# Kernel optimization log

Measured on AMD Instinct MI355X. Metric: run time of the kernel, lower is better.

## Reference

```python
import jax, jax.numpy as jnp
import numpy as np

N_HEAD = 16
D_HEAD = 64
D_MODEL = 1024
QLEN = 1024
BSZ = 4
RLEN = 1024
CONV = 7
SCALE = 1.0 / D_HEAD ** 0.5
NEG = -1e30
EPS = 1e-5


def setup_inputs() -> dict:
    key = jax.random.key(0)
    ks = jax.random.split(key, 14)
    s = 0.02
    inp = {
        "w": jax.random.normal(ks[0], (QLEN, BSZ, D_MODEL), jnp.float32),
        "r": jax.random.normal(ks[1], (RLEN, D_MODEL), jnp.float32),
        "r_w_bias": jax.random.normal(ks[2], (N_HEAD, D_HEAD), jnp.float32) * s,
        "r_r_bias": jax.random.normal(ks[3], (N_HEAD, D_HEAD), jnp.float32) * s,
        "W_qkv": jax.random.normal(ks[4], (3 * N_HEAD * D_HEAD, D_MODEL), jnp.float32) * s,
        "W_r": jax.random.normal(ks[5], (N_HEAD * D_HEAD, D_MODEL), jnp.float32) * s,
        "W_o": jax.random.normal(ks[6], (D_MODEL, N_HEAD * D_HEAD), jnp.float32) * s,
        "conv_wq": jax.random.normal(ks[7], (D_HEAD, D_HEAD, CONV), jnp.float32) * s,
        "conv_bq": jax.random.normal(ks[8], (D_HEAD,), jnp.float32) * s,
        "conv_wk": jax.random.normal(ks[9], (D_HEAD, D_HEAD, CONV), jnp.float32) * s,
        "conv_bk": jax.random.normal(ks[10], (D_HEAD,), jnp.float32) * s,
        "conv_wv": jax.random.normal(ks[11], (D_HEAD, D_HEAD, CONV), jnp.float32) * s,
        "conv_bv": jax.random.normal(ks[12], (D_HEAD,), jnp.float32) * s,
        "ln_gamma": jnp.ones((D_MODEL,), jnp.float32),
        "ln_beta": jnp.zeros((D_MODEL,), jnp.float32),
        # causal mask, True = masked out (original dim==3 branch: [qlen, klen, 1])
        "attn_mask": jnp.triu(jnp.ones((QLEN, QLEN), bool), k=1)[:, :, None],
    }
    return inp


def _conv1d(x, wgt, b):
    # x: [N, C, L], wgt: [O, I, K] (torch Conv1d layout), same padding
    y = jax.lax.conv_general_dilated(x, wgt, (1,), [(CONV // 2, CONV // 2)],
                                     dimension_numbers=("NCH", "OIH", "NCH"))
    return y + b[None, :, None]


def _rel_shift(x):
    # x: [q, k, b, n] -> Transformer-XL relative shift
    q, k, b, n = x.shape
    xp = jnp.concatenate([jnp.zeros((q, 1, b, n), x.dtype), x], axis=1)
    return xp.reshape(k + 1, q, b, n)[1:].reshape(q, k, b, n)


def reference(w, r, r_w_bias, r_r_bias, W_qkv, W_r, W_o,
              conv_wq, conv_bq, conv_wk, conv_bk, conv_wv, conv_bv,
              ln_gamma, ln_beta, attn_mask):
    qlen, bsz, _ = w.shape
    klen = qlen  # mems=None

    heads = jnp.einsum('qbm,hm->qbh', w, W_qkv)  # [q, b, 3*n*d]
    hq, hk, hv = jnp.split(heads, 3, axis=-1)

    def to_conv(x, L):
        # [L, b, n*d] -> [n*b, d, L]
        return x.reshape(L, bsz, N_HEAD, D_HEAD).transpose(2, 1, 3, 0).reshape(N_HEAD * bsz, D_HEAD, L)

    def from_conv(x, L):
        # [n*b, d, L] -> [L, b, n, d]
        return x.reshape(N_HEAD, bsz, D_HEAD, L).transpose(3, 1, 0, 2)

    q_h = from_conv(_conv1d(to_conv(hq, qlen), conv_wq, conv_bq), qlen)
    k_h = from_conv(_conv1d(to_conv(hk, klen), conv_wk, conv_bk), klen)
    v_h = from_conv(_conv1d(to_conv(hv, klen), conv_wv, conv_bv), klen)

    r_head_k = (r @ W_r.T).reshape(-1, N_HEAD, D_HEAD)  # [rlen, n, d]

    AC = jnp.einsum('ibnd,jbnd->ijbn', q_h + r_w_bias, k_h)
    BD = _rel_shift(jnp.einsum('ibnd,jnd->ijbn', q_h + r_r_bias, r_head_k))
    score = (AC + BD) * SCALE
    score = jnp.where(attn_mask[:, :, :, None], NEG, score)

    prob = jax.nn.softmax(score, axis=1)
    vec = jnp.einsum('ijbn,jbnd->ibnd', prob, v_h).reshape(qlen, bsz, N_HEAD * D_HEAD)
    attn_out = vec @ W_o.T

    x = w + attn_out
    mu = jnp.mean(x, axis=-1, keepdims=True)
    var = jnp.mean(jnp.square(x - mu), axis=-1, keepdims=True)
    return (x - mu) / jnp.sqrt(var + EPS) * ln_gamma + ln_beta
```

## Files before the change

kernel.cpp:

```cpp
#include <hip/hip_runtime.h>
#include <math.h>

#define L 1024
#define SCALEF 0.125f
#define NEGF -1e30f

typedef unsigned short u16;
typedef __bf16 bf16x8 __attribute__((ext_vector_type(8)));
typedef float f32x4 __attribute__((ext_vector_type(4)));
typedef unsigned short u16x8 __attribute__((ext_vector_type(8)));
typedef unsigned short u16x4 __attribute__((ext_vector_type(4)));

#define MFMA(a, b, c) __builtin_amdgcn_mfma_f32_16x16x32_bf16(a, b, c, 0, 0, 0)

__device__ inline u16 f2b(float f) {
  union { float f; unsigned u; } v; v.f = f;
  unsigned r = v.u + 0x7fffu + ((v.u >> 16) & 1u);
  return (u16)(r >> 16);
}

__device__ __forceinline__ void ld16(u16* lds, const u16* g) {
  __builtin_amdgcn_global_load_lds((const __attribute__((address_space(1))) unsigned int*)g,
                                   (__attribute__((address_space(3))) unsigned int*)lds, 16, 0, 0);
}

__global__ __launch_bounds__(256) void prep(const float* __restrict__ w, const float* __restrict__ Wqkv,
                                            const float* __restrict__ r, const float* __restrict__ Wr,
                                            const float* __restrict__ Wo,
                                            const float* __restrict__ cwq, const float* __restrict__ cwk,
                                            const float* __restrict__ cwv,
                                            u16* w_bf, u16* wqkv_bf, u16* r_bf, u16* wr_bf, u16* wo_bf,
                                            u16* wTq, u16* wTk, u16* wTv) {
  int i = blockIdx.x * 256 + threadIdx.x;
  if (i < 2621440) {
    const float* s; u16* d; int off;
    if (i < 1048576)      { s = w;    d = w_bf;    off = i; }
    else if (i < 1835008) { s = Wqkv; d = wqkv_bf; off = i - 1048576; }
    else if (i < 2097152) { s = r;    d = r_bf;    off = i - 1835008; }
    else if (i < 2359296) { s = Wr;   d = wr_bf;   off = i - 2097152; }
    else                  { s = Wo;   d = wo_bf;   off = i - 2359296; }
    float4 v = ((const float4*)s)[off];
    u16x4 o = {f2b(v.x), f2b(v.y), f2b(v.z), f2b(v.w)};
    ((u16x4*)d)[off] = o;
  } else {
    int j = i - 2621440;
    if (j < 86016) {
      int z = j / 28672, rem = j % 28672;
      const float* src = z == 0 ? cwq : z == 1 ? cwk : cwv;
      u16* dst = z == 0 ? wTq : z == 1 ? wTk : wTv;
      int tt = rem >> 12, rem2 = rem & 4095;
      int dout = rem2 >> 6, din = rem2 & 63;
      dst[rem] = f2b(src[(dout * 64 + din) * 7 + tt]);
    }
  }
}

template <int OB>
__device__ __forceinline__ void gemm_tile(u16* sA, u16* sB, const u16* A, const u16* B,
                                          void* Cp, int N, int K, int m0, int n0) {
  int t = threadIdx.x;
  int w = t >> 6, lane = t & 63;
  int q4 = lane >> 4, li = lane & 15;
  int mw = (w & 1) << 6, nw = (w >> 1) << 6;
  f32x4 acc[4][4];
#pragma unroll
  for (int i = 0; i < 4; ++i)
#pragma unroll
    for (int j = 0; j < 4; ++j) acc[i][j] = (f32x4){0.f, 0.f, 0.f, 0.f};
  int r0 = t >> 2, c0 = (t & 3) << 3;
  const u16* Ap0 = A + (size_t)(m0 + r0) * K + c0;
  const u16* Ap1 = A + (size_t)(m0 + 64 + r0) * K + c0;
  const u16* Bp0 = B + (size_t)(n0 + r0) * K + c0;
  const u16* Bp1 = B + (size_t)(n0 + 64 + r0) * K + c0;
  u16* sAw = sA + w * 512;
  u16* sBw = sB + w * 512;
  for (int kb = 0; kb < K; kb += 32) {
    __syncthreads();
    ld16(sAw, Ap0 + kb);
    ld16(sAw + 2048, Ap1 + kb);
    ld16(sBw, Bp0 + kb);
    ld16(sBw + 2048, Bp1 + kb);
    __syncthreads();
    bf16x8 fa[4], fb[4];
#pragma unroll
    for (int i = 0; i < 4; ++i) fa[i] = *(const bf16x8*)&sA[(mw + i * 16 + li) * 32 + q4 * 8];
#pragma unroll
    for (int i = 0; i < 4; ++i) fb[i] = *(const bf16x8*)&sB[(nw + i * 16 + li) * 32 + q4 * 8];
#pragma unroll
    for (int mt = 0; mt < 4; ++mt)
#pragma unroll
      for (int nt = 0; nt < 4; ++nt) acc[mt][nt] = MFMA(fa[mt], fb[nt], acc[mt][nt]);
  }
#pragma unroll
  for (int mt = 0; mt < 4; ++mt)
#pragma unroll
    for (int r = 0; r < 4; ++r) {
      size_t row = m0 + mw + mt * 16 + q4 * 4 + r;
      if (OB) {
        u16* C = (u16*)Cp;
#pragma unroll
        for (int nt = 0; nt < 4; ++nt) C[row * N + n0 + nw + nt * 16 + li] = f2b(acc[mt][nt][r]);
      } else {
        float* C = (float*)Cp;
#pragma unroll
        for (int nt = 0; nt < 4; ++nt) C[row * N + n0 + nw + nt * 16 + li] = acc[mt][nt][r];
      }
    }
}

__global__ __launch_bounds__(256) void gemm_stage1(const u16* __restrict__ w_bf, const u16* __restrict__ wqkv_bf,
                                                   u16* __restrict__ heads,
                                                   const u16* __restrict__ r_bf, const u16* __restrict__ wr_bf,
                                                   u16* __restrict__ rhk) {
  __shared__ u16 sA[128 * 32];
  __shared__ u16 sB[128 * 32];
  int id = blockIdx.x;
  if (id < 768) {
    gemm_tile<1>(sA, sB, w_bf, wqkv_bf, heads, 3072, 1024, (id / 24) << 7, (id % 24) << 7);
  } else {
    int j = id - 768;
    gemm_tile<1>(sA, sB, r_bf, wr_bf, rhk, 1024, 1024, (j >> 3) << 7, (j & 7) << 7);
  }
}

__global__ __launch_bounds__(256) void gemm_wo(const u16* __restrict__ A, const u16* __restrict__ B,
                                               float* __restrict__ C) {
  __shared__ u16 sA[64 * 32];
  __shared__ u16 sB[128 * 32];
  int t = threadIdx.x;
  int w = t >> 6, lane = t & 63;
  int q4 = lane >> 4, li = lane & 15;
  int m0 = blockIdx.y << 6, n0 = blockIdx.x << 7;
  int nw = w << 5;
  const int N = 1024, K = 1024;
  f32x4 acc[4][2];
#pragma unroll
  for (int i = 0; i < 4; ++i)
#pragma unroll
    for (int j = 0; j < 2; ++j) acc[i][j] = (f32x4){0.f, 0.f, 0.f, 0.f};
  int r0 = t >> 2, c0 = (t & 3) << 3;
  const u16* Ap = A + (size_t)(m0 + r0) * K + c0;
  const u16* Bp0 = B + (size_t)(n0 + r0) * K + c0;
  const u16* Bp1 = B + (size_t)(n0 + 64 + r0) * K + c0;
  u16* sAw = sA + w * 512;
  u16* sBw = sB + w * 512;
  for (int kb = 0; kb < K; kb += 32) {
    __syncthreads();
    ld16(sAw, Ap + kb);
    ld16(sBw, Bp0 + kb);
    ld16(sBw + 2048, Bp1 + kb);
    __syncthreads();
    bf16x8 fa[4], fb[2];
#pragma unroll
    for (int i = 0; i < 4; ++i) fa[i] = *(const bf16x8*)&sA[(i * 16 + li) * 32 + q4 * 8];
#pragma unroll
    for (int j = 0; j < 2; ++j) fb[j] = *(const bf16x8*)&sB[(nw + j * 16 + li) * 32 + q4 * 8];
#pragma unroll
    for (int mt = 0; mt < 4; ++mt)
#pragma unroll
      for (int nt = 0; nt < 2; ++nt) acc[mt][nt] = MFMA(fa[mt], fb[nt], acc[mt][nt]);
  }
#pragma unroll
  for (int mt = 0; mt < 4; ++mt)
#pragma unroll
    for (int r = 0; r < 4; ++r) {
      size_t row = m0 + mt * 16 + q4 * 4 + r;
#pragma unroll
      for (int nt = 0; nt < 2; ++nt) C[row * N + n0 + nw + nt * 16 + li] = acc[mt][nt][r];
    }
}

__global__ __launch_bounds__(256) void conv3(const u16* __restrict__ x,
                                             const u16* __restrict__ wTq, const u16* __restrict__ wTk,
                                             const u16* __restrict__ wTv,
                                             const float* __restrict__ cbq, const float* __restrict__ cbk,
                                             const float* __restrict__ cbv,
                                             u16* __restrict__ qh, u16* __restrict__ kh, u16* __restrict__ vtg) {
  __shared__ u16 sX[70 * 72];
  int z = blockIdx.z;
  const u16* wT = z == 0 ? wTq : z == 1 ? wTk : wTv;
  const float* bias = z == 0 ? cbq : z == 1 ? cbk : cbv;
  int t = threadIdx.x;
  int w = t >> 6, lane = t & 63;
  int q4 = lane >> 4, li = lane & 15;
  int l0 = blockIdx.x << 6, bn = blockIdx.y;
  int b = bn >> 4, n = bn & 15;
  const u16* xb = x + b * 3072 + z * 1024 + n * 64;
  for (int e = t; e < 560; e += 256) {
    int ro = e >> 3, c = e & 7;
    int l = l0 - 3 + ro;
    u16x8 v = {0, 0, 0, 0, 0, 0, 0, 0};
    if (l >= 0 && l < L) v = *(const u16x8*)(xb + (size_t)l * 12288 + c * 8);
    *(u16x8*)&sX[ro * 72 + c * 8] = v;
  }
  bf16x8 Bw[7][2];
#pragma unroll
  for (int tt = 0; tt < 7; ++tt)
#pragma unroll
    for (int kc = 0; kc < 2; ++kc)
      Bw[tt][kc] = *(const bf16x8*)(wT + (tt * 64 + w * 16 + li) * 64 + kc * 32 + q4 * 8);
  f32x4 acc[4];
#pragma unroll
  for (int i = 0; i < 4; ++i) acc[i] = (f32x4){0.f, 0.f, 0.f, 0.f};
  __syncthreads();
#pragma unroll
  for (int tt = 0; tt < 7; ++tt)
#pragma unroll
    for (int kc = 0; kc < 2; ++kc)
#pragma unroll
      for (int mt = 0; mt < 4; ++mt) {
        bf16x8 a = *(const bf16x8*)&sX[(mt * 16 + li + tt) * 72 + kc * 32 + q4 * 8];
        acc[mt] = MFMA(a, Bw[tt][kc], acc[mt]);
      }
  float bv = bias[w * 16 + li];
  if (z < 2) {
    u16* out = z == 0 ? qh : kh;
#pragma unroll
    for (int mt = 0; mt < 4; ++mt)
#pragma unroll
      for (int r = 0; r < 4; ++r) {
        int l = l0 + mt * 16 + q4 * 4 + r;
        out[(((size_t)l * 4 + b) * 16 + n) * 64 + w * 16 + li] = f2b(acc[mt][r] + bv);
      }
  } else {
    __syncthreads();
#pragma unroll
    for (int mt = 0; mt < 4; ++mt)
#pragma unroll
      for (int r = 0; r < 4; ++r)
        sX[(w * 16 + li) * 72 + mt * 16 + q4 * 4 + r] = f2b(acc[mt][r] + bv);
    __syncthreads();
    int d = t >> 2, ch = t & 3;
    u16x8 v0 = *(u16x8*)&sX[d * 72 + ch * 16];
    u16x8 v1 = *(u16x8*)&sX[d * 72 + ch * 16 + 8];
    u16* dst = vtg + ((size_t)bn * 64 + d) * 1024 + l0 + ch * 16;
    *(u16x8*)dst = v0;
    *(u16x8*)(dst + 8) = v1;
  }
}

__global__ __launch_bounds__(256) void rel_attn(const u16* __restrict__ qh, const u16* __restrict__ kh,
                                                const u16* __restrict__ vt, const u16* __restrict__ rhk,
                                                const float* __restrict__ rwb_, const float* __restrict__ rrb_,
                                                u16* __restrict__ vec) {
  __shared__ u16 sK[64][72];
  __shared__ u16 sVt[64][72];
  __shared__ u16 sR[128][72];
  __shared__ u16 sP[4][16][72];
  int t = threadIdx.x;
  int w = t >> 6, lane = t & 63;
  int q4 = lane >> 4, li = lane & 15;
  int p = blockIdx.x, bn = blockIdx.y;
  int b = bn >> 4, n = bn & 15;
  int base_w = 48 - w * 16;
  const u16* vtb = vt + (size_t)bn * 64 * 1024;
  int er0 = t >> 3, ec = (t & 7) * 8;
  float rwbv[2][8], rrbv[2][8];
#pragma unroll
  for (int kc = 0; kc < 2; ++kc)
#pragma unroll
    for (int j = 0; j < 8; ++j) {
      int d = kc * 32 + q4 * 8 + j;
      rwbv[kc][j] = rwb_[n * 64 + d];
      rrbv[kc][j] = rrb_[n * 64 + d];
    }
  for (int half = 0; half < 2; ++half) {
    int qt = (half == 0) ? p : 15 - p;
    int i0 = qt << 6;
    bf16x8 Aw[2], Ar[2];
    {
      const u16* qrow = qh + (((size_t)(i0 + w * 16 + li) * 4 + b) * 16 + n) * 64;
#pragma unroll
      for (int kc = 0; kc < 2; ++kc) {
        bf16x8 qv = *(const bf16x8*)(qrow + kc * 32 + q4 * 8);
        bf16x8 aw, ar;
#pragma unroll
        for (int j = 0; j < 8; ++j) {
          float qf = (float)qv[j];
          aw[j] = (__bf16)(qf + rwbv[kc][j]);
          ar[j] = (__bf16)(qf + rrbv[kc][j]);
        }
        Aw[kc] = aw;
        Ar[kc] = ar;
      }
    }
    f32x4 accO[4];
#pragma unroll
    for (int i = 0; i < 4; ++i) accO[i] = (f32x4){0.f, 0.f, 0.f, 0.f};
    float lst[4];
#pragma unroll
    for (int r = 0; r < 4; ++r) lst[r] = 0.f;
    int ntile = qt + 1;
    u16x8 pK[2], pV[2], pR[4];
    {
      int j0 = 0, gB = 960 - i0;
#pragma unroll
      for (int i = 0; i < 2; ++i) {
        int row = er0 + i * 32;
        pK[i] = *(const u16x8*)(kh + (((size_t)(j0 + row) * 4 + b) * 16 + n) * 64 + ec);
        pV[i] = *(const u16x8*)(vtb + (size_t)row * 1024 + j0 + ec);
      }
#pragma unroll
      for (int i = 0; i < 4; ++i) {
        int m = er0 + i * 32;
        int g = gB + m;
        if (g > L - 1) g = L - 1;
        pR[i] = *(const u16x8*)(rhk + (size_t)g * 1024 + n * 64 + ec);
      }
    }
    for (int jt = 0; jt < ntile; ++jt) {
      __syncthreads();
#pragma unroll
      for (int i = 0; i < 2; ++i) {
        *(u16x8*)&sK[er0 + i * 32][ec] = pK[i];
        *(u16x8*)&sVt[er0 + i * 32][ec] = pV[i];
      }
#pragma unroll
      for (int i = 0; i < 4; ++i) *(u16x8*)&sR[er0 + i * 32][ec] = pR[i];
      __syncthreads();
      if (jt + 1 < ntile) {
        int j0 = (jt + 1) << 6, gB = 960 - i0 + j0;
#pragma unroll
        for (int i = 0; i < 2; ++i) {
          int row = er0 + i * 32;
          pK[i] = *(const u16x8*)(kh + (((size_t)(j0 + row) * 4 + b) * 16 + n) * 64 + ec);
          pV[i] = *(const u16x8*)(vtb + (size_t)row * 1024 + j0 + ec);
        }
#pragma unroll
        for (int i = 0; i < 4; ++i) {
          int m = er0 + i * 32;
          int g = gB + m;
          if (g > L - 1) g = L - 1;
          pR[i] = *(const u16x8*)(rhk + (size_t)g * 1024 + n * 64 + ec);
        }
      }
      int j0 = jt << 6;
      f32x4 accS[4], accG[5];
#pragma unroll
      for (int i = 0; i < 4; ++i) accS[i] = (f32x4){0.f, 0.f, 0.f, 0.f};
#pragma unroll
      for (int i = 0; i < 5; ++i) accG[i] = (f32x4){0.f, 0.f, 0.f, 0.f};
#pragma unroll
      for (int kc = 0; kc < 2; ++kc) {
#pragma unroll
        for (int nt = 0; nt < 4; ++nt) {
          bf16x8 fk = *(const bf16x8*)&sK[nt * 16 + li][kc * 32 + q4 * 8];
          accS[nt] = MFMA(Aw[kc], fk, accS[nt]);
        }
#pragma unroll
        for (int nt = 0; nt < 5; ++nt) {
          bf16x8 fr = *(const bf16x8*)&sR[base_w + nt * 16 + li][kc * 32 + q4 * 8];
          accG[nt] = MFMA(Ar[kc], fr, accG[nt]);
        }
      }
      float Sv[4][4];
#pragma unroll
      for (int nt = 0; nt < 4; ++nt)
#pragma unroll
        for (int r = 0; r < 4; ++r) {
          int il = q4 * 4 + r;
          int srcc = li + 15 - il;
          int lsrc = (lane & 48) | (srcc & 15);
          float g0 = __shfl(accG[nt][r], lsrc);
          float g1 = __shfl(accG[nt + 1][r], lsrc);
          float g = (srcc < 16) ? g0 : g1;
          Sv[nt][r] = (accS[nt][r] + g) * SCALEF;
        }
      if (jt == qt) {
#pragma unroll
        for (int nt = 0; nt < 4; ++nt)
#pragma unroll
          for (int r = 0; r < 4; ++r)
            if (j0 + nt * 16 + li > i0 + w * 16 + q4 * 4 + r) Sv[nt][r] = NEGF;
      }
      float psum[4];
#pragma unroll
      for (int r = 0; r < 4; ++r) psum[r] = 0.f;
#pragma unroll
      for (int nt = 0; nt < 4; ++nt)
#pragma unroll
        for (int r = 0; r < 4; ++r) {
          float pv = __expf(Sv[nt][r]);
          psum[r] += pv;
          sP[w][q4 * 4 + r][nt * 16 + li] = f2b(pv);
        }
#pragma unroll
      for (int r = 0; r < 4; ++r) {
        float ps = psum[r];
        ps += __shfl_xor(ps, 1);
        ps += __shfl_xor(ps, 2);
        ps += __shfl_xor(ps, 4);
        ps += __shfl_xor(ps, 8);
        lst[r] += ps;
      }
#pragma unroll
      for (int kc = 0; kc < 2; ++kc) {
        bf16x8 ap = *(const bf16x8*)&sP[w][li][kc * 32 + q4 * 8];
#pragma unroll
        for (int nt = 0; nt < 4; ++nt) {
          bf16x8 fv = *(const bf16x8*)&sVt[nt * 16 + li][kc * 32 + q4 * 8];
          accO[nt] = MFMA(ap, fv, accO[nt]);
        }
      }
    }
#pragma unroll
    for (int r = 0; r < 4; ++r) {
      int il = q4 * 4 + r;
      int ig = i0 + w * 16 + il;
      float inv = 1.0f / lst[r];
      u16* orow = vec + (((size_t)ig * 4 + b) * 16 + n) * 64;
#pragma unroll
      for (int nt = 0; nt < 4; ++nt) orow[nt * 16 + li] = f2b(accO[nt][r] * inv);
    }
  }
}

__global__ __launch_bounds__(256) void resid_ln(const float* __restrict__ w,
                                                const float* __restrict__ attn,
                                                const float* __restrict__ gamma,
                                                const float* __restrict__ beta,
                                                float* __restrict__ out) {
  __shared__ float ssum[4], ssq[4];
  int row = blockIdx.x, t = threadIdx.x;
  float4 xw = *(const float4*)&w[(size_t)row * 1024 + t * 4];
  float4 xa = *(const float4*)&attn[(size_t)row * 1024 + t * 4];
  float4 x = make_float4(xw.x + xa.x, xw.y + xa.y, xw.z + xa.z, xw.w + xa.w);
  float s = x.x + x.y + x.z + x.w;
  float sq = x.x * x.x + x.y * x.y + x.z * x.z + x.w * x.w;
#pragma unroll
  for (int off = 32; off > 0; off >>= 1) {
    s += __shfl_down(s, off);
    sq += __shfl_down(sq, off);
  }
  int wid = t >> 6;
  if ((t & 63) == 0) { ssum[wid] = s; ssq[wid] = sq; }
  __syncthreads();
  s = ssum[0] + ssum[1] + ssum[2] + ssum[3];
  sq = ssq[0] + ssq[1] + ssq[2] + ssq[3];
  float mean = s * (1.0f / 1024.0f);
  float var = sq * (1.0f / 1024.0f) - mean * mean;
  float rstd = rsqrtf(var + 1e-5f);
  float4 g = *(const float4*)&gamma[t * 4];
  float4 bb = *(const float4*)&beta[t * 4];
  float4 o;
  o.x = (x.x - mean) * rstd * g.x + bb.x;
  o.y = (x.y - mean) * rstd * g.y + bb.y;
  o.z = (x.z - mean) * rstd * g.z + bb.z;
  o.w = (x.w - mean) * rstd * g.w + bb.w;
  *(float4*)&out[(size_t)row * 1024 + t * 4] = o;
}

extern "C" void kernel_launch(void* const* d_in, const int* in_sizes, int n_in,
                              void* d_out, int out_size, void* d_ws, size_t ws_size,
                              hipStream_t stream) {
  const float* w     = (const float*)d_in[0];
  const float* r     = (const float*)d_in[1];
  const float* rwb   = (const float*)d_in[2];
  const float* rrb   = (const float*)d_in[3];
  const float* W_qkv = (const float*)d_in[4];
  const float* W_r   = (const float*)d_in[5];
  const float* W_o   = (const float*)d_in[6];
  const float* cwq   = (const float*)d_in[7];
  const float* cbq   = (const float*)d_in[8];
  const float* cwk   = (const float*)d_in[9];
  const float* cbk   = (const float*)d_in[10];
  const float* cwv   = (const float*)d_in[11];
  const float* cbv   = (const float*)d_in[12];
  const float* gamma = (const float*)d_in[13];
  const float* beta  = (const float*)d_in[14];
  float* outp = (float*)d_out;

  char* wsb = (char*)d_ws;
  u16*   heads   = (u16*)(wsb);
  u16*   vec     = (u16*)(wsb);
  float* attnf   = (float*)(wsb + 8388608);
  u16*   qh      = (u16*)(wsb + 25165824);
  u16*   kh      = (u16*)(wsb + 33554432);
  u16*   rhk     = (u16*)(wsb + 50331648);
  u16*   w_bf    = (u16*)(wsb + 52428800);
  u16*   wqkv_bf = (u16*)(wsb + 60817408);
  u16*   r_bf    = (u16*)(wsb + 67108864);
  u16*   wr_bf   = (u16*)(wsb + 69206016);
  u16*   wo_bf   = (u16*)(wsb + 71303168);
  u16*   wTq     = (u16*)(wsb + 73400320);
  u16*   wTk     = (u16*)(wsb + 73457664);
  u16*   wTv     = (u16*)(wsb + 73515008);
  u16*   vt      = (u16*)(wsb + 73572352);

  dim3 blk(256);
  prep<<<10576, blk, 0, stream>>>(w, W_qkv, r, W_r, W_o, cwq, cwk, cwv,
                                  w_bf, wqkv_bf, r_bf, wr_bf, wo_bf, wTq, wTk, wTv);
  gemm_stage1<<<832, blk, 0, stream>>>(w_bf, wqkv_bf, heads, r_bf, wr_bf, rhk);
  conv3<<<dim3(16, 64, 3), blk, 0, stream>>>(heads, wTq, wTk, wTv, cbq, cbk, cbv, qh, kh, vt);
  rel_attn<<<dim3(8, 64), blk, 0, stream>>>(qh, kh, vt, rhk, rwb, rrb, vec);
  gemm_wo<<<dim3(8, 64), blk, 0, stream>>>(vec, wo_bf, attnf);
  resid_ln<<<4096, blk, 0, stream>>>(w, attnf, gamma, beta, outp);
}
```

Measured before the change: 270.0 us.

## Double-buffer LDS tiles in the projection GEMMs to overlap loads with MFMA

Both GEMM kernels (the QKV/R projection tile and the output projection) now keep two LDS buffers. The next k-slice is prefetched with global_load_lds into the other buffer while MFMAs run on the current one, which removes one of the two barriers per k-step. The aim is to hide global-to-LDS load latency behind compute. The cost is twice the shared memory per block, which may lower occupancy. If the compiler inserts a full vmcnt wait before the LDS reads, the overlap may not happen.

```diff
diff --git a/kernel.cpp b/kernel.cpp
--- a/kernel.cpp
+++ b/kernel.cpp
@@ -72,24 +72,35 @@
   const u16* Ap1 = A + (size_t)(m0 + 64 + r0) * K + c0;
   const u16* Bp0 = B + (size_t)(n0 + r0) * K + c0;
   const u16* Bp1 = B + (size_t)(n0 + 64 + r0) * K + c0;
-  u16* sAw = sA + w * 512;
-  u16* sBw = sB + w * 512;
+  int wo512 = w * 512;
+  ld16(sA + wo512, Ap0);
+  ld16(sA + wo512 + 2048, Ap1);
+  ld16(sB + wo512, Bp0);
+  ld16(sB + wo512 + 2048, Bp1);
+  int cur = 0;
   for (int kb = 0; kb < K; kb += 32) {
     __syncthreads();
-    ld16(sAw, Ap0 + kb);
-    ld16(sAw + 2048, Ap1 + kb);
-    ld16(sBw, Bp0 + kb);
-    ld16(sBw + 2048, Bp1 + kb);
-    __syncthreads();
+    int nxt = cur ^ 1;
+    if (kb + 32 < K) {
+      u16* nA = sA + nxt * 4096;
+      u16* nB = sB + nxt * 4096;
+      ld16(nA + wo512, Ap0 + kb + 32);
+      ld16(nA + wo512 + 2048, Ap1 + kb + 32);
+      ld16(nB + wo512, Bp0 + kb + 32);
+      ld16(nB + wo512 + 2048, Bp1 + kb + 32);
+    }
+    const u16* cA = sA + cur * 4096;
+    const u16* cB = sB + cur * 4096;
     bf16x8 fa[4], fb[4];
 #pragma unroll
-    for (int i = 0; i < 4; ++i) fa[i] = *(const bf16x8*)&sA[(mw + i * 16 + li) * 32 + q4 * 8];
-#pragma unroll
-    for (int i = 0; i < 4; ++i) fb[i] = *(const bf16x8*)&sB[(nw + i * 16 + li) * 32 + q4 * 8];
+    for (int i = 0; i < 4; ++i) fa[i] = *(const bf16x8*)&cA[(mw + i * 16 + li) * 32 + q4 * 8];
+#pragma unroll
+    for (int i = 0; i < 4; ++i) fb[i] = *(const bf16x8*)&cB[(nw + i * 16 + li) * 32 + q4 * 8];
 #pragma unroll
     for (int mt = 0; mt < 4; ++mt)
 #pragma unroll
       for (int nt = 0; nt < 4; ++nt) acc[mt][nt] = MFMA(fa[mt], fb[nt], acc[mt][nt]);
+    cur = nxt;
   }
 #pragma unroll
   for (int mt = 0; mt < 4; ++mt)
@@ -112,8 +123,8 @@
                                                    u16* __restrict__ heads,
                                                    const u16* __restrict__ r_bf, const u16* __restrict__ wr_bf,
                                                    u16* __restrict__ rhk) {
-  __shared__ u16 sA[128 * 32];
-  __shared__ u16 sB[128 * 32];
+  __shared__ u16 sA[2 * 128 * 32];
+  __shared__ u16 sB[2 * 128 * 32];
   int id = blockIdx.x;
   if (id < 768) {
     gemm_tile<1>(sA, sB, w_bf, wqkv_bf, heads, 3072, 1024, (id / 24) << 7, (id % 24) << 7);
@@ -125,8 +136,8 @@
 
 __global__ __launch_bounds__(256) void gemm_wo(const u16* __restrict__ A, const u16* __restrict__ B,
                                                float* __restrict__ C) {
-  __shared__ u16 sA[64 * 32];
-  __shared__ u16 sB[128 * 32];
+  __shared__ u16 sA[2 * 64 * 32];
+  __shared__ u16 sB[2 * 128 * 32];
   int t = threadIdx.x;
   int w = t >> 6, lane = t & 63;
   int q4 = lane >> 4, li = lane & 15;
@@ -142,23 +153,33 @@
   const u16* Ap = A + (size_t)(m0 + r0) * K + c0;
   const u16* Bp0 = B + (size_t)(n0 + r0) * K + c0;
   const u16* Bp1 = B + (size_t)(n0 + 64 + r0) * K + c0;
-  u16* sAw = sA + w * 512;
-  u16* sBw = sB + w * 512;
+  int wo512 = w * 512;
+  ld16(sA + wo512, Ap);
+  ld16(sB + wo512, Bp0);
+  ld16(sB + wo512 + 2048, Bp1);
+  int cur = 0;
   for (int kb = 0; kb < K; kb += 32) {
     __syncthreads();
-    ld16(sAw, Ap + kb);
-    ld16(sBw, Bp0 + kb);
-    ld16(sBw + 2048, Bp1 + kb);
-    __syncthreads();
+    int nxt = cur ^ 1;
+    if (kb + 32 < K) {
+      u16* nA = sA + nxt * 2048;
+      u16* nB = sB + nxt * 4096;
+      ld16(nA + wo512, Ap + kb + 32);
+      ld16(nB + wo512, Bp0 + kb + 32);
+      ld16(nB + wo512 + 2048, Bp1 + kb + 32);
+    }
+    const u16* cA = sA + cur * 2048;
+    const u16* cB = sB + cur * 4096;
     bf16x8 fa[4], fb[2];
 #pragma unroll
-    for (int i = 0; i < 4; ++i) fa[i] = *(const bf16x8*)&sA[(i * 16 + li) * 32 + q4 * 8];
-#pragma unroll
-    for (int j = 0; j < 2; ++j) fb[j] = *(const bf16x8*)&sB[(nw + j * 16 + li) * 32 + q4 * 8];
+    for (int i = 0; i < 4; ++i) fa[i] = *(const bf16x8*)&cA[(i * 16 + li) * 32 + q4 * 8];
+#pragma unroll
+    for (int j = 0; j < 2; ++j) fb[j] = *(const bf16x8*)&cB[(nw + j * 16 + li) * 32 + q4 * 8];
 #pragma unroll
     for (int mt = 0; mt < 4; ++mt)
 #pragma unroll
       for (int nt = 0; nt < 2; ++nt) acc[mt][nt] = MFMA(fa[mt], fb[nt], acc[mt][nt]);
+    cur = nxt;
   }
 #pragma unroll
   for (int mt = 0; mt < 4; ++mt)
```

Result: no change. 265.2 us (-1.8%).
